# Performance work log

Hardware: AMD Instinct MI355X
Metric: run time of the kernel (lower is better)

The kernel has to match this reference:

```python
import jax, jax.numpy as jnp
import numpy as np
import math

B, T, H, D = 4, 2048, 16, 64
C = H * D            # d_model = 1024
FF = 4096            # mlp_hidden_dim
N_LAYERS = 12
EPS = 1e-5


def setup_inputs() -> dict:
    key = jax.random.key(0)
    ks = jax.random.split(key, 8)
    res_scale = 1.0 / math.sqrt(2 * N_LAYERS)
    std_c = math.sqrt(2.0 / C)
    std_ff = math.sqrt(2.0 / FF)
    return {
        "x": jax.random.normal(ks[0], (B, T, C), jnp.float32),
        "ln1_w": jnp.ones((C,), jnp.float32),
        "ln1_b": jnp.zeros((C,), jnp.float32),
        # weights stored [in, out] (transposed vs torch nn.Linear.weight)
        "w_qkv": jax.random.normal(ks[1], (C, 3 * C), jnp.float32) * std_c,
        "b_qkv": jnp.zeros((3 * C,), jnp.float32),
        "w_o": jax.random.normal(ks[2], (C, C), jnp.float32) * std_c * res_scale,
        "b_o": jnp.zeros((C,), jnp.float32),
        "ln2_w": jnp.ones((C,), jnp.float32),
        "ln2_b": jnp.zeros((C,), jnp.float32),
        "w_fc": jax.random.normal(ks[3], (C, FF), jnp.float32) * std_c,
        "b_fc": jnp.zeros((FF,), jnp.float32),
        "w_out": jax.random.normal(ks[4], (FF, C), jnp.float32) * std_ff * res_scale,
        "b_out": jnp.zeros((C,), jnp.float32),
    }


def _layer_norm(x, w, b):
    m = jnp.mean(x, axis=-1, keepdims=True)
    v = jnp.mean(jnp.square(x - m), axis=-1, keepdims=True)
    return (x - m) * jax.lax.rsqrt(v + EPS) * w + b


def reference(x, ln1_w, ln1_b, w_qkv, b_qkv, w_o, b_o, ln2_w, ln2_b, w_fc, b_fc, w_out, b_out):
    Bx, Tx, Cx = x.shape
    # attention
    qkv = _layer_norm(x, ln1_w, ln1_b) @ w_qkv + b_qkv          # [B,T,3C]
    q, k, v = jnp.split(qkv, 3, axis=-1)
    q = q.reshape(Bx, Tx, H, D)
    k = k.reshape(Bx, Tx, H, D)
    v = v.reshape(Bx, Tx, H, D)
    att = jnp.einsum("bqhd,bkhd->bhqk", q, k) / math.sqrt(D)    # [B,H,T,T]
    mask = jnp.tril(jnp.ones((Tx, Tx), dtype=bool))
    att = jnp.where(mask, att, -jnp.inf)
    att = jax.nn.softmax(att, axis=-1)
    y = jnp.einsum("bhqk,bkhd->bqhd", att, v).reshape(Bx, Tx, Cx)
    x = x + y @ w_o + b_o
    # mlp (torch F.gelu default = exact erf gelu)
    h = jax.nn.gelu(_layer_norm(x, ln2_w, ln2_b) @ w_fc + b_fc, approximate=False)
    x = x + h @ w_out + b_out
    return x
```

## Files before the change

### kernel.cpp

```cpp
#include <hip/hip_runtime.h>
#include <hip/hip_bf16.h>
#include <cstdint>


#define B_ 4
#define T_ 2048
#define H_ 16
#define D_ 64
#define C_ 1024
#define FF_ 4096
#define M_ (B_ * T_)
#define QKV_N (3 * C_)

typedef __bf16 bf16x8 __attribute__((ext_vector_type(8)));
typedef __bf16 bf16x4 __attribute__((ext_vector_type(4)));
typedef float floatx4 __attribute__((ext_vector_type(4)));

#define MFMA16(a, b, c) __builtin_amdgcn_mfma_f32_16x16x32_bf16(a, b, c, 0, 0, 0)

__device__ __forceinline__ void gload16(const void* g, void* l) {
  __builtin_amdgcn_global_load_lds(
      (const __attribute__((address_space(1))) void*)g,
      (__attribute__((address_space(3))) void*)l, 16, 0, 0);
}

__device__ __forceinline__ void lds_fence() {
  asm volatile("s_waitcnt lgkmcnt(0)" ::: "memory");
}

__device__ __forceinline__ float gelu_f(float x) {
  const float k1 = 2.3021178518f;
  const float ck = 0.1029410426f;
  const float y = x * __builtin_fmaf(x * x, ck, k1);
  const float t = __builtin_amdgcn_exp2f(y);
  return x - x * __builtin_amdgcn_rcpf(t + 1.0f);
}

__global__ __launch_bounds__(256) void convert_transpose(
    const float* __restrict__ w, __bf16* __restrict__ wt, int K, int N) {
  __shared__ float tile[32][33];
  const int n0 = blockIdx.x * 32, k0 = blockIdx.y * 32;
  const int tx = threadIdx.x & 31, ty = threadIdx.x >> 5;
#pragma unroll
  for (int i = 0; i < 4; ++i)
    tile[ty + i * 8][tx] = w[(size_t)(k0 + ty + i * 8) * N + n0 + tx];
  __syncthreads();
#pragma unroll
  for (int i = 0; i < 4; ++i)
    wt[(size_t)(n0 + ty + i * 8) * K + k0 + tx] = (__bf16)tile[tx][ty + i * 8];
}

__global__ __launch_bounds__(256) void ln_kernel(
    const float* __restrict__ x, const float* __restrict__ w,
    const float* __restrict__ b, __bf16* __restrict__ out) {
  __shared__ float red[4];
  const int row = blockIdx.x, tid = threadIdx.x;
  const float4 v = ((const float4*)(x + (size_t)row * C_))[tid];
  float s = v.x + v.y + v.z + v.w;
#pragma unroll
  for (int off = 1; off < 64; off <<= 1) s += __shfl_xor(s, off, 64);
  if ((tid & 63) == 0) red[tid >> 6] = s;
  __syncthreads();
  const float mean = (red[0] + red[1] + red[2] + red[3]) * (1.0f / C_);
  __syncthreads();
  const float dx = v.x - mean, dy = v.y - mean, dz = v.z - mean, dw = v.w - mean;
  float s2 = dx * dx + dy * dy + dz * dz + dw * dw;
#pragma unroll
  for (int off = 1; off < 64; off <<= 1) s2 += __shfl_xor(s2, off, 64);
  if ((tid & 63) == 0) red[tid >> 6] = s2;
  __syncthreads();
  const float var = (red[0] + red[1] + red[2] + red[3]) * (1.0f / C_);
  const float rstd = rsqrtf(var + 1e-5f);
  const float4 wv = ((const float4*)w)[tid];
  const float4 bv = ((const float4*)b)[tid];
  bf16x4 o;
  o[0] = (__bf16)(dx * rstd * wv.x + bv.x);
  o[1] = (__bf16)(dy * rstd * wv.y + bv.y);
  o[2] = (__bf16)(dz * rstd * wv.z + bv.z);
  o[3] = (__bf16)(dw * rstd * wv.w + bv.w);
  *(bf16x4*)(out + (size_t)row * C_ + tid * 4) = o;
}

__device__ __forceinline__ void swizzle_mn(int gx, int gy, int* bm, int* bn) {
  const int linear = blockIdx.y * gx + blockIdx.x;
  const int xcd = linear & 7, idx = linear >> 3;
  const int band = gy >> 3;
  const int per_grp = band * 8;
  const int g = idx / per_grp, rem = idx % per_grp;
  *bm = xcd * band + rem % band;
  *bn = g * 8 + rem / band;
}

template <bool GELU, bool RESID, bool OUTBF16>
__global__ __launch_bounds__(256, 2) void gemm_kernel(
    const __bf16* __restrict__ A, const __bf16* __restrict__ BT,
    const float* __restrict__ bias, const float* __restrict__ resid,
    float* __restrict__ outF, __bf16* __restrict__ outB, int M, int N, int K) {
  __shared__ __bf16 As[128 * 64];
  __shared__ __bf16 Bs[128 * 64];
  const int tid = threadIdx.x;
  const int wave = tid >> 6, lane = tid & 63;
  const int lane15 = lane & 15, quad = lane >> 4;
  const int r7 = lane15 & 7;

  int bm, bn;
  swizzle_mn(gridDim.x, gridDim.y, &bm, &bn);
  const int m0 = bm * 128, n0 = bn * 128;
  const int wm = (wave >> 1) * 64, wn = (wave & 1) * 64;

  const int srow = lane >> 3;
  const int gc8 = (lane & 7) ^ srow;

  floatx4 acc[4][4] = {};

  for (int k0 = 0; k0 < K; k0 += 64) {
#pragma unroll
    for (int t = 0; t < 4; ++t) {
      const int row = wave * 32 + t * 8;
      gload16(A + (size_t)(m0 + row + srow) * K + k0 + gc8 * 8, &As[row * 64]);
      gload16(BT + (size_t)(n0 + row + srow) * K + k0 + gc8 * 8, &Bs[row * 64]);
    }
    __syncthreads();
#pragma unroll
    for (int kk8 = 0; kk8 < 8; kk8 += 4) {
      bf16x8 af[4], bfr[4];
#pragma unroll
      for (int i = 0; i < 4; ++i) {
        af[i] = *(const bf16x8*)
            &As[(wm + i * 16 + lane15) * 64 + (((kk8 + quad) ^ r7) << 3)];
        bfr[i] = *(const bf16x8*)
            &Bs[(wn + i * 16 + lane15) * 64 + (((kk8 + quad) ^ r7) << 3)];
      }
#pragma unroll
      for (int i = 0; i < 4; ++i)
#pragma unroll
        for (int j = 0; j < 4; ++j) acc[i][j] = MFMA16(af[i], bfr[j], acc[i][j]);
    }
    __syncthreads();
  }

#pragma unroll
  for (int mi = 0; mi < 4; ++mi) {
    const int row = m0 + wm + mi * 16 + quad * 4;
#pragma unroll
    for (int ni = 0; ni < 4; ++ni) {
      const int col = n0 + wn + ni * 16 + lane15;
      const float bsum = bias[col];
#pragma unroll
      for (int r = 0; r < 4; ++r) {
        const size_t idx2 = (size_t)(row + r) * N + col;
        float v = acc[mi][ni][r] + bsum;
        if (GELU) v = gelu_f(v);
        if (RESID) v += resid[idx2];
        if (OUTBF16) outB[idx2] = (__bf16)v;
        else outF[idx2] = v;
      }
    }
  }
}

template <bool GELU, bool RESID, bool OUTBF16>
__global__ __launch_bounds__(256, 4) void gemm_n64_kernel(
    const __bf16* __restrict__ A, const __bf16* __restrict__ BT,
    const float* __restrict__ bias, const float* __restrict__ resid,
    float* __restrict__ outF, __bf16* __restrict__ outB, int M, int N, int K) {
  __shared__ __bf16 As[128 * 64];
  __shared__ __bf16 Bs[64 * 64];
  const int tid = threadIdx.x;
  const int wave = tid >> 6, lane = tid & 63;
  const int lane15 = lane & 15, quad = lane >> 4;
  const int r7 = lane15 & 7;

  int bm, bn;
  swizzle_mn(gridDim.x, gridDim.y, &bm, &bn);
  const int m0 = bm * 128, n0 = bn * 64;
  const int wm = (wave >> 1) * 64, wn = (wave & 1) * 32;

  const int srow = lane >> 3;
  const int gc8 = (lane & 7) ^ srow;

  floatx4 acc[4][2] = {};

  for (int k0 = 0; k0 < K; k0 += 64) {
#pragma unroll
    for (int t = 0; t < 4; ++t) {
      const int row = wave * 32 + t * 8;
      gload16(A + (size_t)(m0 + row + srow) * K + k0 + gc8 * 8, &As[row * 64]);
    }
#pragma unroll
    for (int t = 0; t < 2; ++t) {
      const int row = wave * 16 + t * 8;
      gload16(BT + (size_t)(n0 + row + srow) * K + k0 + gc8 * 8, &Bs[row * 64]);
    }
    __syncthreads();
#pragma unroll
    for (int kk8 = 0; kk8 < 8; kk8 += 4) {
      bf16x8 af[4], bfr[2];
#pragma unroll
      for (int i = 0; i < 4; ++i)
        af[i] = *(const bf16x8*)
            &As[(wm + i * 16 + lane15) * 64 + (((kk8 + quad) ^ r7) << 3)];
#pragma unroll
      for (int j = 0; j < 2; ++j)
        bfr[j] = *(const bf16x8*)
            &Bs[(wn + j * 16 + lane15) * 64 + (((kk8 + quad) ^ r7) << 3)];
#pragma unroll
      for (int i = 0; i < 4; ++i)
#pragma unroll
        for (int j = 0; j < 2; ++j) acc[i][j] = MFMA16(af[i], bfr[j], acc[i][j]);
    }
    __syncthreads();
  }

#pragma unroll
  for (int mi = 0; mi < 4; ++mi) {
    const int row = m0 + wm + mi * 16 + quad * 4;
#pragma unroll
    for (int ni = 0; ni < 2; ++ni) {
      const int col = n0 + wn + ni * 16 + lane15;
      const float bsum = bias[col];
#pragma unroll
      for (int r = 0; r < 4; ++r) {
        const size_t idx2 = (size_t)(row + r) * N + col;
        float v = acc[mi][ni][r] + bsum;
        if (GELU) v = gelu_f(v);
        if (RESID) v += resid[idx2];
        if (OUTBF16) outB[idx2] = (__bf16)v;
        else outF[idx2] = v;
      }
    }
  }
}

#define PT_S 72
#define VT_S 72
__global__ __launch_bounds__(256, 4) void attn_kernel(
    const __bf16* __restrict__ qkv, __bf16* __restrict__ y) {
  const int linear = blockIdx.x;
  const int xcd = linear & 7, idx = linear >> 3;
  const int pair = idx & 15;
  const int bh = xcd * 8 + (idx >> 4);
  const int b = bh >> 4, h = bh & 15;

  const int tid = threadIdx.x, wave = tid >> 6, lane = tid & 63;
  const int lane15 = lane & 15, quad = lane >> 4;
  __shared__ __bf16 K0[2][64 * 32];
  __shared__ __bf16 K1[2][64 * 32];
  __shared__ __bf16 Vt[64 * VT_S];
  __shared__ __bf16 Pt[4][16 * PT_S];

  const int krow_loc = lane >> 2;
  const int kdc = (lane & 3) * 8;
  const int v_kvp = tid & 31;
  const int v_dgrp = tid >> 5;
  const float QSCALE = 0.125f * 1.44269504088896f;

  const int qt_of[2] = {pair, 31 - pair};

  bf16x8 onesf;
#pragma unroll
  for (int j = 0; j < 8; ++j) onesf[j] = (__bf16)1.0f;

  bf16x8 vr0, vr1;
  int g = 0;

  {
    const size_t gk =
        (size_t)(b * T_ + wave * 16 + krow_loc) * QKV_N + C_ + h * 64 + kdc;
    gload16(qkv + gk, &K0[0][wave * 16 * 32]);
    gload16(qkv + gk + 32, &K1[0][wave * 16 * 32]);
    const __bf16* vsrc = qkv + (size_t)(b * T_ + 2 * v_kvp) * QKV_N +
                         2 * C_ + h * 64 + v_dgrp * 8;
    vr0 = *(const bf16x8*)vsrc;
    vr1 = *(const bf16x8*)(vsrc + QKV_N);
  }

#pragma unroll
  for (int seg = 0; seg < 2; ++seg) {
    const int qt = qt_of[seg];
    const int qrow0 = qt * 64 + wave * 16;
    const int tq = qrow0 + lane15;

    bf16x8 qf0, qf1;
    {
      const size_t base =
          (size_t)(b * T_ + qrow0 + lane15) * QKV_N + h * 64 + quad * 8;
      const bf16x8 r0 = *(const bf16x8*)(qkv + base);
      const bf16x8 r1 = *(const bf16x8*)(qkv + base + 32);
#pragma unroll
      for (int j = 0; j < 8; ++j) {
        qf0[j] = (__bf16)((float)r0[j] * QSCALE);
        qf1[j] = (__bf16)((float)r1[j] * QSCALE);
      }
    }

    floatx4 o[4] = {};
    floatx4 o4 = {0.f, 0.f, 0.f, 0.f};

    const int ntiles = qt + 1;
    for (int kvt = 0; kvt < ntiles; ++kvt) {
      const int buf = g & 1;
      const int c0 = kvt * 64;
      __syncthreads();
#pragma unroll
      for (int j = 0; j < 8; ++j) {
        union { __bf16 hh[2]; uint32_t u; } pk;
        pk.hh[0] = vr0[j];
        pk.hh[1] = vr1[j];
        *(uint32_t*)&Vt[(v_dgrp * 8 + j) * VT_S + 2 * v_kvp] = pk.u;
      }
      __syncthreads();

      if (!(seg == 1 && kvt + 1 >= ntiles)) {
        const int nkvt = (kvt + 1 >= ntiles) ? 0 : kvt + 1;
        const int nc0 = nkvt * 64;
        const int nbuf = (g + 1) & 1;
        const size_t gk = (size_t)(b * T_ + nc0 + wave * 16 + krow_loc) * QKV_N +
                          C_ + h * 64 + kdc;
        gload16(qkv + gk, &K0[nbuf][wave * 16 * 32]);
        gload16(qkv + gk + 32, &K1[nbuf][wave * 16 * 32]);
        const __bf16* vsrc = qkv + (size_t)(b * T_ + nc0 + 2 * v_kvp) * QKV_N +
                             2 * C_ + h * 64 + v_dgrp * 8;
        vr0 = *(const bf16x8*)vsrc;
        vr1 = *(const bf16x8*)(vsrc + QKV_N);
      }

#pragma unroll
      for (int nt = 0; nt < 4; ++nt) {
        const bf16x8 kf0 =
            *(const bf16x8*)&K0[buf][(nt * 16 + lane15) * 32 + quad * 8];
        const bf16x8 kf1 =
            *(const bf16x8*)&K1[buf][(nt * 16 + lane15) * 32 + quad * 8];
        floatx4 s = {0.f, 0.f, 0.f, 0.f};
        s = MFMA16(kf0, qf0, s);
        s = MFMA16(kf1, qf1, s);
        const int tk0 = c0 + nt * 16 + quad * 4;
        bf16x4 pk4;
        if (kvt == qt) {
#pragma unroll
          for (int r = 0; r < 4; ++r) {
            const float sv = (tk0 + r <= tq) ? s[r] : -1e30f;
            pk4[r] = (__bf16)__builtin_amdgcn_exp2f(sv);
          }
        } else {
#pragma unroll
          for (int r = 0; r < 4; ++r)
            pk4[r] = (__bf16)__builtin_amdgcn_exp2f(s[r]);
        }
        *(bf16x4*)&Pt[wave][lane15 * PT_S + nt * 16 + quad * 4] = pk4;
      }
      lds_fence();

#pragma unroll
      for (int half = 0; half < 2; ++half) {
        const bf16x8 pf =
            *(const bf16x8*)&Pt[wave][lane15 * PT_S + half * 32 + quad * 8];
#pragma unroll
        for (int dt = 0; dt < 4; ++dt) {
          const bf16x8 vf =
              *(const bf16x8*)&Vt[(dt * 16 + lane15) * VT_S + half * 32 + quad * 8];
          o[dt] = MFMA16(pf, vf, o[dt]);
        }
        o4 = MFMA16(pf, onesf, o4);
      }
      ++g;
    }

#pragma unroll
    for (int r = 0; r < 4; ++r) {
      const int tqo = qrow0 + quad * 4 + r;
      const float inv = 1.0f / o4[r];
#pragma unroll
      for (int dt = 0; dt < 4; ++dt)
        y[(size_t)(b * T_ + tqo) * C_ + h * 64 + dt * 16 + lane15] =
            (__bf16)(o[dt][r] * inv);
    }
  }
}

extern "C" void kernel_launch(void* const* d_in, const int* in_sizes, int n_in,
                              void* d_out, int out_size, void* d_ws,
                              size_t ws_size, hipStream_t stream) {
  const float* x     = (const float*)d_in[0];
  const float* ln1_w = (const float*)d_in[1];
  const float* ln1_b = (const float*)d_in[2];
  const float* w_qkv = (const float*)d_in[3];
  const float* b_qkv = (const float*)d_in[4];
  const float* w_o   = (const float*)d_in[5];
  const float* b_o   = (const float*)d_in[6];
  const float* ln2_w = (const float*)d_in[7];
  const float* ln2_b = (const float*)d_in[8];
  const float* w_fc  = (const float*)d_in[9];
  const float* b_fc  = (const float*)d_in[10];
  const float* w_out = (const float*)d_in[11];
  const float* b_out = (const float*)d_in[12];

  char* ws = (char*)d_ws;
  __bf16* wqkvT = (__bf16*)(ws + 0);
  __bf16* woT   = (__bf16*)(ws + 6291456);
  __bf16* wfcT  = (__bf16*)(ws + 8388608);
  __bf16* woutT = (__bf16*)(ws + 16777216);
  __bf16* xn    = (__bf16*)(ws + 25165824);
  __bf16* qkv   = (__bf16*)(ws + 41943040);
  __bf16* yb    = (__bf16*)(ws + 92274688);
  float*  x1    = (float*)(ws + 109051904);
  __bf16* hb    = (__bf16*)(ws + 142606336);

  convert_transpose<<<dim3(QKV_N / 32, C_ / 32), 256, 0, stream>>>(w_qkv, wqkvT, C_, QKV_N);
  convert_transpose<<<dim3(C_ / 32, C_ / 32), 256, 0, stream>>>(w_o, woT, C_, C_);
  convert_transpose<<<dim3(FF_ / 32, C_ / 32), 256, 0, stream>>>(w_fc, wfcT, C_, FF_);
  convert_transpose<<<dim3(C_ / 32, FF_ / 32), 256, 0, stream>>>(w_out, woutT, FF_, C_);

  ln_kernel<<<M_, 256, 0, stream>>>(x, ln1_w, ln1_b, xn);
  gemm_kernel<false, false, true><<<dim3(QKV_N / 128, M_ / 128), 256, 0, stream>>>(
      xn, wqkvT, b_qkv, nullptr, nullptr, qkv, M_, QKV_N, C_);
  attn_kernel<<<1024, 256, 0, stream>>>(qkv, yb);
  gemm_n64_kernel<false, true, false><<<dim3(C_ / 64, M_ / 128), 256, 0, stream>>>(
      yb, woT, b_o, x, x1, nullptr, M_, C_, C_);
  ln_kernel<<<M_, 256, 0, stream>>>(x1, ln2_w, ln2_b, xn);
  gemm_kernel<true, false, true><<<dim3(FF_ / 128, M_ / 128), 256, 0, stream>>>(
      xn, wfcT, b_fc, nullptr, nullptr, hb, M_, FF_, C_);
  gemm_n64_kernel<false, true, false><<<dim3(C_ / 64, M_ / 128), 256, 0, stream>>>(
      hb, woutT, b_out, x1, (float*)d_out, nullptr, M_, C_, FF_);
}
```

Before: 475.0 us.

## Add 256x256 tiled 8-wave GEMM with staged prefetch for QKV and FC projections

Adds a new 512-thread GEMM kernel with 256x256 output tiles, double-buffered LDS filled by direct global-to-LDS loads, and quarter-tile staging interleaved with MFMA groups under barriers and raised wave priority. It replaces the 128x128 GEMM for the QKV and FC projections, and moves the output projection from the N64 kernel to the 128x128 kernel. Larger tiles increase operand reuse per load, but they also use a lot of LDS and allow only one block per CU, and the M=8192 grids are coarse, so tail effects may appear.

```diff
diff --git a/kernel.cpp b/kernel.cpp
--- a/kernel.cpp
+++ b/kernel.cpp
@@ -26,6 +26,18 @@
 
 __device__ __forceinline__ void lds_fence() {
   asm volatile("s_waitcnt lgkmcnt(0)" ::: "memory");
+}
+
+__device__ __forceinline__ void bar() {
+  asm volatile("" ::: "memory");
+  __builtin_amdgcn_s_barrier();
+  asm volatile("" ::: "memory");
+}
+__device__ __forceinline__ void waitvm4() {
+  asm volatile("s_waitcnt vmcnt(4)" ::: "memory");
+}
+__device__ __forceinline__ void waitvm0() {
+  asm volatile("s_waitcnt vmcnt(0)" ::: "memory");
 }
 
 __device__ __forceinline__ float gelu_f(float x) {
@@ -230,6 +242,139 @@
       }
     }
   }
+}
+
+#define LOADB(BF, nh, buf)                                                     \
+  do {                                                                         \
+    _Pragma("unroll") for (int ni = 0; ni < 2; ++ni) {                         \
+      const int row_ = wc * 64 + (nh) * 32 + ni * 16 + lane15;                 \
+      _Pragma("unroll") for (int ks = 0; ks < 2; ++ks)                         \
+          BF[ni][ks] = *(const bf16x8*)&Bs[buf][row_ * 64 +                    \
+                                               (((ks * 4 + quad) ^ r7) << 3)]; \
+    }                                                                          \
+  } while (0)
+
+#define MFMA_QUAD(mh, nh, BF)                                                  \
+  do {                                                                         \
+    __builtin_amdgcn_s_setprio(1);                                             \
+    _Pragma("unroll") for (int mi = 0; mi < 4; ++mi)                           \
+        _Pragma("unroll") for (int ni = 0; ni < 2; ++ni)                       \
+            _Pragma("unroll") for (int ks = 0; ks < 2; ++ks)                   \
+                acc[mh][mi][(nh) * 2 + ni] = MFMA16(                           \
+                    af[mi][ks], BF[ni][ks], acc[mh][mi][(nh) * 2 + ni]);       \
+    __builtin_amdgcn_s_setprio(0);                                             \
+  } while (0)
+
+template <bool GELU>
+__global__ __launch_bounds__(512, 1) void gemm256_kernel(
+    const __bf16* __restrict__ A, const __bf16* __restrict__ BT,
+    const float* __restrict__ bias, __bf16* __restrict__ outB,
+    int M, int N, int K) {
+  __shared__ __bf16 As[2][256 * 64];
+  __shared__ __bf16 Bs[2][256 * 64];
+  const int tid = threadIdx.x;
+  const int wave = tid >> 6, lane = tid & 63;
+  const int lane15 = lane & 15, quad = lane >> 4, r7 = lane15 & 7;
+  const int wr = wave >> 2, wc = wave & 3;
+  const int srow = lane >> 3, gc8 = (lane & 7) ^ srow;
+
+  const int linear = blockIdx.y * gridDim.x + blockIdx.x;
+  const int xcd = linear & 7, idx = linear >> 3;
+  const int band = gridDim.y >> 3;
+  const int bm = xcd * band + idx % band;
+  const int bn = idx / band;
+  const int m0 = bm * 256, n0 = bn * 256;
+  const int NT = K >> 6;
+
+  const __bf16* Ab = A + (size_t)(m0 + srow) * K + gc8 * 8;
+  const __bf16* Bb = BT + (size_t)(n0 + srow) * K + gc8 * 8;
+  const int chunk = wave * 2;
+
+  auto stageA = [&](int q, int t, int buf) {
+#pragma unroll
+    for (int i = 0; i < 2; ++i) {
+      const int c = chunk + i;
+      const int rr = q * 64 + ((c >> 3) * 128) + (c & 7) * 8;
+      gload16(Ab + (size_t)rr * K + t * 64, &As[buf][rr * 64]);
+    }
+  };
+  auto stageB = [&](int q, int t, int buf) {
+#pragma unroll
+    for (int i = 0; i < 2; ++i) {
+      const int c = chunk + i;
+      const int rr = q * 32 + ((c >> 2) * 64) + (c & 3) * 8;
+      gload16(Bb + (size_t)rr * K + t * 64, &Bs[buf][rr * 64]);
+    }
+  };
+
+  bf16x8 af[4][2], b0f[2][2], b1f[2][2];
+  auto loadA = [&](int mh, int buf) {
+#pragma unroll
+    for (int mi = 0; mi < 4; ++mi) {
+      const int row = wr * 128 + mh * 64 + mi * 16 + lane15;
+#pragma unroll
+      for (int ks = 0; ks < 2; ++ks)
+        af[mi][ks] = *(const bf16x8*)
+            &As[buf][row * 64 + (((ks * 4 + quad) ^ r7) << 3)];
+    }
+  };
+
+  floatx4 acc[2][4][4] = {};
+
+  stageA(0, 0, 0);
+  stageA(1, 0, 0);
+  stageB(0, 0, 0);
+  stageB(1, 0, 0);
+  stageA(0, 1, 1);
+  stageB(1, 1, 1);
+  waitvm4();
+  bar();
+
+  for (int t = 0; t < NT; ++t) {
+    const int buf = t & 1, nbuf = buf ^ 1;
+    if (t + 1 < NT) stageA(1, t + 1, nbuf);
+    loadA(0, buf);
+    LOADB(b0f, 0, buf);
+    bar();
+    MFMA_QUAD(0, 0, b0f);
+    bar();
+    if (t + 1 < NT) stageB(0, t + 1, nbuf);
+    LOADB(b1f, 1, buf);
+    bar();
+    MFMA_QUAD(0, 1, b1f);
+    bar();
+    if (t + 2 < NT) stageA(0, t + 2, buf);
+    loadA(1, buf);
+    bar();
+    MFMA_QUAD(1, 1, b1f);
+    bar();
+    if (t + 2 < NT) stageB(1, t + 2, buf);
+    bar();
+    MFMA_QUAD(1, 0, b0f);
+    if (t + 1 < NT) {
+      if (t + 2 < NT) waitvm4();
+      else waitvm0();
+      bar();
+    }
+  }
+
+#pragma unroll
+  for (int mh = 0; mh < 2; ++mh)
+#pragma unroll
+    for (int mi = 0; mi < 4; ++mi) {
+      const int row = m0 + wr * 128 + mh * 64 + mi * 16 + quad * 4;
+#pragma unroll
+      for (int ni = 0; ni < 4; ++ni) {
+        const int col = n0 + wc * 64 + ni * 16 + lane15;
+        const float bsum = bias[col];
+#pragma unroll
+        for (int r = 0; r < 4; ++r) {
+          float v = acc[mh][mi][ni][r] + bsum;
+          if (GELU) v = gelu_f(v);
+          outB[(size_t)(row + r) * N + col] = (__bf16)v;
+        }
+      }
+    }
 }
 
 #define PT_S 72
@@ -412,14 +557,14 @@
   convert_transpose<<<dim3(C_ / 32, FF_ / 32), 256, 0, stream>>>(w_out, woutT, FF_, C_);
 
   ln_kernel<<<M_, 256, 0, stream>>>(x, ln1_w, ln1_b, xn);
-  gemm_kernel<false, false, true><<<dim3(QKV_N / 128, M_ / 128), 256, 0, stream>>>(
-      xn, wqkvT, b_qkv, nullptr, nullptr, qkv, M_, QKV_N, C_);
+  gemm256_kernel<false><<<dim3(QKV_N / 256, M_ / 256), 512, 0, stream>>>(
+      xn, wqkvT, b_qkv, qkv, M_, QKV_N, C_);
   attn_kernel<<<1024, 256, 0, stream>>>(qkv, yb);
   gemm_n64_kernel<false, true, false><<<dim3(C_ / 64, M_ / 128), 256, 0, stream>>>(
       yb, woT, b_o, x, x1, nullptr, M_, C_, C_);
   ln_kernel<<<M_, 256, 0, stream>>>(x1, ln2_w, ln2_b, xn);
-  gemm_kernel<true, false, true><<<dim3(FF_ / 128, M_ / 128), 256, 0, stream>>>(
-      xn, wfcT, b_fc, nullptr, nullptr, hb, M_, FF_, C_);
-  gemm_n64_kernel<false, true, false><<<dim3(C_ / 64, M_ / 128), 256, 0, stream>>>(
+  gemm256_kernel<true><<<dim3(FF_ / 256, M_ / 256), 512, 0, stream>>>(
+      xn, wfcT, b_fc, hb, M_, FF_, C_);
+  gemm_kernel<false, true, false><<<dim3(C_ / 128, M_ / 128), 256, 0, stream>>>(
       hb, woutT, b_out, x1, (float*)d_out, nullptr, M_, C_, FF_);
 }
```

Result: slower. 515.9 us (+8.6%).
